# Performance work log

Measured on AMD Instinct MI355X. Metric: run time of the kernel, lower is better.

Reference implementation:

```python
import jax, jax.numpy as jnp
import numpy as np

S, B, D, H, F = 2048, 4, 256, 8, 2048
HD = D // H


def _ln(x, g, b, eps=1e-5):
    mu = jnp.mean(x, axis=-1, keepdims=True)
    var = jnp.var(x, axis=-1, keepdims=True)
    return (x - mu) * jax.lax.rsqrt(var + eps) * g + b


def setup_inputs() -> dict:
    key = jax.random.key(0)
    ks = jax.random.split(key, 8)
    s = lambda fan: 1.0 / np.sqrt(fan)
    return {
        "features": jax.random.normal(ks[0], (S, B, D), jnp.float32),
        "ln_g": jnp.ones((D,), jnp.float32),
        "ln_b": jnp.zeros((D,), jnp.float32),
        "in_proj_w": jax.random.normal(ks[1], (3 * D, D), jnp.float32) * s(D),
        "in_proj_b": jnp.zeros((3 * D,), jnp.float32),
        "out_proj_w": jax.random.normal(ks[2], (D, D), jnp.float32) * s(D),
        "out_proj_b": jnp.zeros((D,), jnp.float32),
        "w1": jax.random.normal(ks[3], (F, D), jnp.float32) * s(D),
        "b1": jnp.zeros((F,), jnp.float32),
        "w2": jax.random.normal(ks[4], (D, F), jnp.float32) * s(F),
        "b2": jnp.zeros((D,), jnp.float32),
    }


def _attn_tanh_relu(x, in_proj_w, in_proj_b, out_proj_w, out_proj_b):
    # x: (S, B, D). Standard MHA projections, but relu(tanh(.)) replaces softmax.
    qkv = x @ in_proj_w.T + in_proj_b            # (S, B, 3D)
    q, k, v = jnp.split(qkv, 3, axis=-1)
    q = q.reshape(S, B, H, HD) * (1.0 / np.sqrt(HD))
    k = k.reshape(S, B, H, HD)
    v = v.reshape(S, B, H, HD)
    scores = jnp.einsum("sbhd,tbhd->bhst", q, k)  # (B, H, S, S)
    w = jax.nn.relu(jnp.tanh(scores))
    out = jnp.einsum("bhst,tbhd->sbhd", w, v).reshape(S, B, D)
    return out @ out_proj_w.T + out_proj_b


def reference(features, ln_g, ln_b, in_proj_w, in_proj_b, out_proj_w, out_proj_b, w1, b1, w2, b2):
    ln_x = _ln(features, ln_g, ln_b)
    attn = _attn_tanh_relu(ln_x, in_proj_w, in_proj_b, out_proj_w, out_proj_b)
    r1 = _ln(ln_x + attn, ln_g, ln_b)
    ff = jax.nn.relu(r1 @ w1.T + b1) @ w2.T + b2
    return _ln(r1 + ff, ln_g, ln_b)
```

## Files before the change

kernel.cpp:

```cpp
#include <hip/hip_runtime.h>
#include <hip/hip_bf16.h>

#define SS 2048
#define BB 4
#define DD 256
#define HH 8
#define HDD 32
#define FFD 2048
#define MM (SS*BB)

typedef __attribute__((ext_vector_type(8))) __bf16 bf16x8;
typedef __attribute__((ext_vector_type(2))) __bf16 bf16x2;
typedef __attribute__((ext_vector_type(8))) short short8;
typedef __attribute__((ext_vector_type(4))) short short4v;
typedef __attribute__((ext_vector_type(4))) float f32x4;
typedef __attribute__((ext_vector_type(16))) float f32x16;
typedef __attribute__((ext_vector_type(2))) unsigned uint2v;
typedef __attribute__((ext_vector_type(4))) unsigned uint4v;

__device__ __forceinline__ unsigned short f2bf(float f) {
  union { float f; unsigned u; } v; v.f = f;
  unsigned r = v.u + 0x7fffu + ((v.u >> 16) & 1u);
  return (unsigned short)(r >> 16);
}

__device__ __forceinline__ unsigned pk2(float a, float b) {
  bf16x2 t; t[0] = (__bf16)a; t[1] = (__bf16)b;
  return __builtin_bit_cast(unsigned, t);
}

__device__ __forceinline__ void gload16(const void* g, void* l) {
  __builtin_amdgcn_global_load_lds(
      (const __attribute__((address_space(1))) void*)g,
      (__attribute__((address_space(3))) void*)l, 16, 0, 0);
}

__global__ __launch_bounds__(256)
void cvt_all(const float* __restrict__ a, const float* __restrict__ b,
             const float* __restrict__ c, const float* __restrict__ d,
             short* __restrict__ oa, short* __restrict__ ob,
             short* __restrict__ oc, short* __restrict__ od) {
  const int which = blockIdx.y;
  const float* in; short* out; int n4;
  if (which == 0)      { in = a; out = oa; n4 = 768 * 256 / 4; }
  else if (which == 1) { in = b; out = ob; n4 = 256 * 256 / 4; }
  else if (which == 2) { in = c; out = oc; n4 = 2048 * 256 / 4; }
  else                 { in = d; out = od; n4 = 2048 * 256 / 4; }
  const int i = blockIdx.x * 256 + threadIdx.x;
  if (i < n4) {
    float4 x = ((const float4*)in)[i];
    short4v o = { (short)f2bf(x.x), (short)f2bf(x.y), (short)f2bf(x.z), (short)f2bf(x.w) };
    ((short4v*)out)[i] = o;
  }
}

template<int NIN, int WF, int WBF>
__global__ __launch_bounds__(256)
void ln_kernel(const float* __restrict__ xa, const float* __restrict__ xb,
               const float* __restrict__ xc,
               const float* __restrict__ gam, const float* __restrict__ bet,
               float* __restrict__ outf, short* __restrict__ outb)
{
  const int w = threadIdx.x >> 6, l = threadIdx.x & 63;
  const size_t row = (size_t)blockIdx.x * 4 + w;
  float4 x = *(const float4*)&xa[row * 256 + l * 4];
  if (NIN >= 2) {
    const float4 y = *(const float4*)&xb[row * 256 + l * 4];
    x.x += y.x; x.y += y.y; x.z += y.z; x.w += y.w;
  }
  if (NIN >= 3) {
    const float4 y = *(const float4*)&xc[row * 256 + l * 4];
    x.x += y.x; x.y += y.y; x.z += y.z; x.w += y.w;
  }
  float sum = x.x + x.y + x.z + x.w;
  float sq  = x.x*x.x + x.y*x.y + x.z*x.z + x.w*x.w;
#pragma unroll
  for (int off = 32; off > 0; off >>= 1) {
    sum += __shfl_xor(sum, off);
    sq  += __shfl_xor(sq, off);
  }
  const float mu = sum * (1.f / 256.f);
  const float rs = rsqrtf(sq * (1.f / 256.f) - mu * mu + 1e-5f);
  const float4 g4 = *(const float4*)&gam[l * 4];
  const float4 b4 = *(const float4*)&bet[l * 4];
  const float y0 = (x.x - mu) * rs * g4.x + b4.x;
  const float y1 = (x.y - mu) * rs * g4.y + b4.y;
  const float y2 = (x.z - mu) * rs * g4.z + b4.z;
  const float y3 = (x.w - mu) * rs * g4.w + b4.w;
  if (WF) {
    float4 o; o.x = y0; o.y = y1; o.z = y2; o.w = y3;
    *(float4*)&outf[row * 256 + l * 4] = o;
  }
  if (WBF) {
    short4v o = { (short)f2bf(y0), (short)f2bf(y1), (short)f2bf(y2), (short)f2bf(y3) };
    *(short4v*)&outb[row * 256 + l * 4] = o;
  }
}

template<int EPI, int BM, int BN, int KW>
__global__ __launch_bounds__(256)
void gemm_bt(const short* __restrict__ A, const short* __restrict__ W,
             const float* __restrict__ bias, void* __restrict__ out,
             void* __restrict__ out2, int K, int N, int Ksub)
{
  __shared__ short sA[2][BM * 64];
  __shared__ short sB[2][BN * 64];
  const int tid = threadIdx.x;
  const int l  = tid & 63;
  const int w  = tid >> 6;
  const int wr = w >> 1, wc = w & 1;
  const int lr = l & 15, lg = l >> 4;
  const long row0 = (long)blockIdx.y * BM;
  const long col0 = (long)blockIdx.x * BN;
  const int kz = blockIdx.z;
  const int kbeg = kz * Ksub;
  const int ldsw = (tid & ~63) * 16;
  constexpr int MR = BM / 32, NR = BN / 32;
  f32x4 acc[MR][NR] = {};
  const int nt = Ksub / 64;

  auto stage = [&](int buf, int k0) {
#pragma unroll
    for (int i = 0; i < BM / 32; i++) {
      const int o = (i * 256 + tid) * 16;
      const int r = o >> 7;
      const int cg = ((o >> 4) & 7) ^ (r & 7);
      gload16((const char*)A + ((row0 + r) * (long)K + k0) * 2 + cg * 16,
              (char*)sA[buf] + i * 4096 + ldsw);
    }
    const long wstride = KW ? KW : K;
    const long wk = KW ? (k0 & (KW - 1)) : k0;
#pragma unroll
    for (int i = 0; i < BN / 32; i++) {
      const int o = (i * 256 + tid) * 16;
      const int r = o >> 7;
      const int cg = ((o >> 4) & 7) ^ (r & 7);
      gload16((const char*)W + ((col0 + r) * wstride + wk) * 2 + cg * 16,
              (char*)sB[buf] + i * 4096 + ldsw);
    }
  };

  stage(0, kbeg);
  __syncthreads();
  int cur = 0;
  for (int t = 0; t < nt; t++) {
    if (t + 1 < nt) stage(cur ^ 1, kbeg + (t + 1) * 64);
    bf16x8 af[MR][2], bw[NR][2];
#pragma unroll
    for (int m = 0; m < MR; m++)
#pragma unroll
      for (int kk = 0; kk < 2; kk++) {
        const int row = wr * (BM/2) + m * 16 + lr;
        af[m][kk] = *(const bf16x8*)&sA[cur][row * 64 + (((kk*4 + lg) ^ (lr & 7)) * 8)];
      }
#pragma unroll
    for (int n = 0; n < NR; n++)
#pragma unroll
      for (int kk = 0; kk < 2; kk++) {
        const int row = wc * (BN/2) + n * 16 + lr;
        bw[n][kk] = *(const bf16x8*)&sB[cur][row * 64 + (((kk*4 + lg) ^ (lr & 7)) * 8)];
      }
#pragma unroll
    for (int kk = 0; kk < 2; kk++)
#pragma unroll
      for (int m = 0; m < MR; m++)
#pragma unroll
        for (int n = 0; n < NR; n++)
          acc[m][n] = __builtin_amdgcn_mfma_f32_16x16x32_bf16(af[m][kk], bw[n][kk], acc[m][n], 0, 0, 0);
    __syncthreads();
    cur ^= 1;
  }

#pragma unroll
  for (int m = 0; m < MR; m++) {
    const long rbase = row0 + wr * (BM/2) + m * 16 + lg * 4;
#pragma unroll
    for (int n = 0; n < NR; n++) {
      const long c = col0 + wc * (BN/2) + n * 16 + lr;
      const float bv = (EPI == 3 && kz) ? 0.f : bias[c];
#pragma unroll
      for (int j = 0; j < 4; j++) {
        const long r = rbase + j;
        float val = acc[m][n][j] + bv;
        if (EPI == 0) {
          const int part = (int)(c >> 8);
          const int cc = (int)(c & 255);
          const int h = cc >> 5, hd = cc & 31;
          const int bi = (int)(r & 3);
          const int s = (int)(r >> 2);
          const int bh = bi * HH + h;
          if (part == 0) val *= 0.51006972771029396f;
          size_t idx;
          if (part == 2) {
            idx = (size_t)2 * (MM * DD) + (size_t)bh * (SS * HDD)
                + (size_t)(s >> 3) * (HDD * 8) + hd * 8 + (s & 7);
          } else {
            idx = (size_t)part * (MM * DD) + ((size_t)bh * SS + s) * HDD + hd;
          }
          ((short*)out)[idx] = (short)f2bf(val);
        } else if (EPI == 1) {
          ((float*)out)[(size_t)r * N + c] = val;
        } else if (EPI == 2) {
          ((short*)out)[(size_t)r * N + c] = (short)f2bf(fmaxf(val, 0.f));
        } else {
          float* op = kz ? (float*)out2 : (float*)out;
          op[(size_t)r * N + c] = val;
        }
      }
    }
  }
}

__global__ __launch_bounds__(256, 4)
void attn_kernel(const short* __restrict__ Qb, const short* __restrict__ Kb,
                 const short* __restrict__ Vb, short* __restrict__ Aout)
{
  const int tid = threadIdx.x;
  const int l = tid & 63, w = tid >> 6;
  const int q32 = l & 31, hf = l >> 5;
  const int i = blockIdx.x;
  const int j = i >> 3;
  const int p = (i & 7) + 8 * (j >> 6);
  const int rem = j & 63;
  const int q0 = (rem >> 2) * 128 + w * 32;
  const int kz = rem & 3;
  const int kbeg = kz * (SS / 4);
  const int kend = kbeg + SS / 4;
  const size_t base = (size_t)p * SS * HDD;
  const short* Q  = Qb + base;
  const short* Kp = Kb + base;
  const short* Vp = Vb + base;

  const short* qrow = &Q[(size_t)(q0 + q32) * HDD];
  const bf16x8 qf0 = *(const bf16x8*)&qrow[hf * 8];
  const bf16x8 qf1 = *(const bf16x8*)&qrow[16 + hf * 8];

  const f32x16 fzero = {};
  f32x16 accA = {}, accB = {};

  auto loadK = [&](int t0, bf16x8* kf) {
    const short* kr = &Kp[(size_t)(t0 + q32) * HDD];
    kf[0] = *(const bf16x8*)&kr[hf * 8];
    kf[1] = *(const bf16x8*)&kr[16 + hf * 8];
  };
  auto loadV = [&](int t0, bf16x8* vf) {
    const short* vb = &Vp[(size_t)((t0 >> 3) + hf) * (HDD * 8) + q32 * 8];
    vf[0] = *(const bf16x8*)&vb[0];
    vf[1] = *(const bf16x8*)&vb[2 * (HDD * 8)];
  };

  auto step = [&](const bf16x8* kf, const bf16x8* vf, f32x16& acc) {
    f32x16 s = __builtin_amdgcn_mfma_f32_32x32x16_bf16(kf[0], qf0, fzero, 0, 0, 0);
    s = __builtin_amdgcn_mfma_f32_32x32x16_bf16(kf[1], qf1, s, 0, 0, 0);
    float pv[16];
#pragma unroll
    for (int r = 0; r < 16; r++) {
      const float e = __builtin_amdgcn_exp2f(s[r]);
      pv[r] = fmaxf(1.f - 2.f * __builtin_amdgcn_rcpf(e + 1.f), 0.f);
    }
    unsigned X0 = pk2(pv[0], pv[1]),   X1 = pk2(pv[2], pv[3]);
    unsigned X2 = pk2(pv[4], pv[5]),   X3 = pk2(pv[6], pv[7]);
    unsigned X4 = pk2(pv[8], pv[9]),   X5 = pk2(pv[10], pv[11]);
    unsigned X6 = pk2(pv[12], pv[13]), X7 = pk2(pv[14], pv[15]);
    uint2v r02 = __builtin_amdgcn_permlane32_swap(X0, X2, false, false);
    uint2v r13 = __builtin_amdgcn_permlane32_swap(X1, X3, false, false);
    uint2v r46 = __builtin_amdgcn_permlane32_swap(X4, X6, false, false);
    uint2v r57 = __builtin_amdgcn_permlane32_swap(X5, X7, false, false);
    const uint4v f0 = { r02[0], r13[0], r02[1], r13[1] };
    const uint4v f1 = { r46[0], r57[0], r46[1], r57[1] };
    const bf16x8 pa0 = __builtin_bit_cast(bf16x8, f0);
    const bf16x8 pa1 = __builtin_bit_cast(bf16x8, f1);
    acc = __builtin_amdgcn_mfma_f32_32x32x16_bf16(pa0, vf[0], acc, 0, 0, 0);
    acc = __builtin_amdgcn_mfma_f32_32x32x16_bf16(pa1, vf[1], acc, 0, 0, 0);
  };

  bf16x8 kA[2], vA[2], kB[2], vB[2];
  loadK(kbeg, kA); loadV(kbeg, vA);
  for (int t0 = kbeg; t0 < kend; t0 += 64) {
    loadK(t0 + 32, kB); loadV(t0 + 32, vB);
    step(kA, vA, accA);
    const int tn = (t0 + 64 < kend) ? t0 + 64 : kbeg;
    loadK(tn, kA); loadV(tn, vA);
    step(kB, vB, accB);
  }

  const int bi = p >> 3, hh = p & 7;
  const size_t colo = (size_t)kz * DD + (size_t)hh * HDD + q32;
#pragma unroll
  for (int r = 0; r < 16; r++) {
    const int crow = (r & 3) + 8 * (r >> 2) + 4 * hf;
    Aout[((size_t)(q0 + crow) * BB + bi) * (4 * DD) + colo] =
        (short)f2bf(accA[r] + accB[r]);
  }
}

extern "C" void kernel_launch(void* const* d_in, const int* in_sizes, int n_in,
                              void* d_out, int out_size, void* d_ws, size_t ws_size,
                              hipStream_t stream) {
  const float* features   = (const float*)d_in[0];
  const float* ln_g       = (const float*)d_in[1];
  const float* ln_b       = (const float*)d_in[2];
  const float* in_proj_w  = (const float*)d_in[3];
  const float* in_proj_b  = (const float*)d_in[4];
  const float* out_proj_w = (const float*)d_in[5];
  const float* out_proj_b = (const float*)d_in[6];
  const float* w1 = (const float*)d_in[7];
  const float* b1 = (const float*)d_in[8];
  const float* w2 = (const float*)d_in[9];
  const float* b2 = (const float*)d_in[10];

  char* ws = (char*)d_ws;
  const size_t MB = 1024 * 1024;
  float* lnx_f  = (float*)(ws + 0);
  short* lnx_b  = (short*)(ws + 8 * MB);
  short* qkv    = (short*)(ws + 12 * MB);
  short* aprt   = (short*)(ws + 24 * MB);
  float* proj   = (float*)(ws + 12 * MB);
  short* r1_b   = (short*)(ws + 20 * MB);
  float* r1_f   = (float*)(ws + 24 * MB);
  short* h1     = (short*)(ws + 32 * MB);
  float* ffb    = (float*)(ws + 12 * MB);
  float* ffp1   = (float*)(ws + 0);
  short* wqkv_b = (short*)(ws + 64 * MB);
  short* wout_b = wqkv_b + 768 * 256;
  short* w1_b   = wout_b + 256 * 256;
  short* w2_b   = w1_b + 2048 * 256;

  cvt_all<<<dim3(512, 4), 256, 0, stream>>>(in_proj_w, out_proj_w, w1, w2,
                                            wqkv_b, wout_b, w1_b, w2_b);

  ln_kernel<1, 1, 1><<<2048, 256, 0, stream>>>(features, nullptr, nullptr, ln_g, ln_b, lnx_f, lnx_b);

  gemm_bt<0, 128, 64, 0><<<dim3(12, 64, 1), 256, 0, stream>>>(lnx_b, wqkv_b, in_proj_b, qkv, nullptr, 256, 768, 256);

  attn_kernel<<<dim3(2048, 1, 1), 256, 0, stream>>>(qkv, qkv + 2097152, qkv + 2 * 2097152, aprt);

  gemm_bt<1, 64, 64, 256><<<dim3(4, 128, 1), 256, 0, stream>>>(aprt, wout_b, out_proj_b, proj, nullptr, 1024, 256, 1024);

  ln_kernel<2, 1, 1><<<2048, 256, 0, stream>>>(lnx_f, proj, nullptr, ln_g, ln_b, r1_f, r1_b);

  gemm_bt<2, 128, 128, 0><<<dim3(16, 64, 1), 256, 0, stream>>>(r1_b, w1_b, b1, h1, nullptr, 256, 2048, 256);

  gemm_bt<3, 128, 64, 0><<<dim3(4, 64, 2), 256, 0, stream>>>(h1, w2_b, b2, ffb, ffp1, 2048, 256, 1024);

  ln_kernel<3, 1, 0><<<2048, 256, 0, stream>>>(r1_f, ffb, ffp1, ln_g, ln_b, (float*)d_out, nullptr);
}
```

Before: 132.0 us.

## Fuse weight conversion with first LayerNorm, halve attention key split, bf16 FFN partials

Merges the weight-conversion kernel and the first LayerNorm into one launch, removing a kernel boundary. The attention key-split factor drops from 4 to 2, which halves the partial-output buffer and the K dimension of the out-projection GEMM. The second FFN GEMM now writes its split-K partials as bf16 instead of fp32, and the final LayerNorm reads them as bf16. This cuts memory traffic and launch overhead, at the cost of fewer attention blocks (less parallelism) and extra bf16 rounding on the FFN partial sums.

```diff
diff --git a/kernel.cpp b/kernel.cpp
--- a/kernel.cpp
+++ b/kernel.cpp
@@ -24,6 +24,12 @@
   return (unsigned short)(r >> 16);
 }
 
+__device__ __forceinline__ float bf2f(short s) {
+  union { float f; unsigned u; } v;
+  v.u = ((unsigned)(unsigned short)s) << 16;
+  return v.f;
+}
+
 __device__ __forceinline__ unsigned pk2(float a, float b) {
   bf16x2 t; t[0] = (__bf16)a; t[1] = (__bf16)b;
   return __builtin_bit_cast(unsigned, t);
@@ -36,28 +42,57 @@
 }
 
 __global__ __launch_bounds__(256)
-void cvt_all(const float* __restrict__ a, const float* __restrict__ b,
-             const float* __restrict__ c, const float* __restrict__ d,
-             short* __restrict__ oa, short* __restrict__ ob,
-             short* __restrict__ oc, short* __restrict__ od) {
-  const int which = blockIdx.y;
-  const float* in; short* out; int n4;
-  if (which == 0)      { in = a; out = oa; n4 = 768 * 256 / 4; }
-  else if (which == 1) { in = b; out = ob; n4 = 256 * 256 / 4; }
-  else if (which == 2) { in = c; out = oc; n4 = 2048 * 256 / 4; }
-  else                 { in = d; out = od; n4 = 2048 * 256 / 4; }
-  const int i = blockIdx.x * 256 + threadIdx.x;
-  if (i < n4) {
-    float4 x = ((const float4*)in)[i];
-    short4v o = { (short)f2bf(x.x), (short)f2bf(x.y), (short)f2bf(x.z), (short)f2bf(x.w) };
-    ((short4v*)out)[i] = o;
-  }
-}
-
-template<int NIN, int WF, int WBF>
+void cvt_ln(const float* __restrict__ a, const float* __restrict__ b,
+            const float* __restrict__ c, const float* __restrict__ d,
+            short* __restrict__ oa, short* __restrict__ ob,
+            short* __restrict__ oc, short* __restrict__ od,
+            const float* __restrict__ feat,
+            const float* __restrict__ gam, const float* __restrict__ bet,
+            float* __restrict__ lnf, short* __restrict__ lnb)
+{
+  const int y = blockIdx.y;
+  if (y < 4) {
+    const float* in; short* out; int n4;
+    if (y == 0)      { in = a; out = oa; n4 = 768 * 256 / 4; }
+    else if (y == 1) { in = b; out = ob; n4 = 256 * 256 / 4; }
+    else if (y == 2) { in = c; out = oc; n4 = 2048 * 256 / 4; }
+    else             { in = d; out = od; n4 = 2048 * 256 / 4; }
+    const int i = blockIdx.x * 256 + threadIdx.x;
+    if (i < n4) {
+      float4 x = ((const float4*)in)[i];
+      short4v o = { (short)f2bf(x.x), (short)f2bf(x.y), (short)f2bf(x.z), (short)f2bf(x.w) };
+      ((short4v*)out)[i] = o;
+    }
+    return;
+  }
+  const int w = threadIdx.x >> 6, l = threadIdx.x & 63;
+  const size_t row = (size_t)blockIdx.x * 4 + w;
+  float4 x = *(const float4*)&feat[row * 256 + l * 4];
+  float sum = x.x + x.y + x.z + x.w;
+  float sq  = x.x*x.x + x.y*x.y + x.z*x.z + x.w*x.w;
+#pragma unroll
+  for (int off = 32; off > 0; off >>= 1) {
+    sum += __shfl_xor(sum, off);
+    sq  += __shfl_xor(sq, off);
+  }
+  const float mu = sum * (1.f / 256.f);
+  const float rs = rsqrtf(sq * (1.f / 256.f) - mu * mu + 1e-5f);
+  const float4 g4 = *(const float4*)&gam[l * 4];
+  const float4 b4 = *(const float4*)&bet[l * 4];
+  const float y0 = (x.x - mu) * rs * g4.x + b4.x;
+  const float y1 = (x.y - mu) * rs * g4.y + b4.y;
+  const float y2 = (x.z - mu) * rs * g4.z + b4.z;
+  const float y3 = (x.w - mu) * rs * g4.w + b4.w;
+  float4 o; o.x = y0; o.y = y1; o.z = y2; o.w = y3;
+  *(float4*)&lnf[row * 256 + l * 4] = o;
+  short4v ob2 = { (short)f2bf(y0), (short)f2bf(y1), (short)f2bf(y2), (short)f2bf(y3) };
+  *(short4v*)&lnb[row * 256 + l * 4] = ob2;
+}
+
+template<int NIN, int WF, int WBF, int BFI>
 __global__ __launch_bounds__(256)
-void ln_kernel(const float* __restrict__ xa, const float* __restrict__ xb,
-               const float* __restrict__ xc,
+void ln_kernel(const float* __restrict__ xa, const void* __restrict__ xb,
+               const void* __restrict__ xc,
                const float* __restrict__ gam, const float* __restrict__ bet,
                float* __restrict__ outf, short* __restrict__ outb)
 {
@@ -65,12 +100,22 @@
   const size_t row = (size_t)blockIdx.x * 4 + w;
   float4 x = *(const float4*)&xa[row * 256 + l * 4];
   if (NIN >= 2) {
-    const float4 y = *(const float4*)&xb[row * 256 + l * 4];
-    x.x += y.x; x.y += y.y; x.z += y.z; x.w += y.w;
+    if (BFI) {
+      const short4v yb = *(const short4v*)&((const short*)xb)[row * 256 + l * 4];
+      x.x += bf2f(yb[0]); x.y += bf2f(yb[1]); x.z += bf2f(yb[2]); x.w += bf2f(yb[3]);
+    } else {
+      const float4 yv = *(const float4*)&((const float*)xb)[row * 256 + l * 4];
+      x.x += yv.x; x.y += yv.y; x.z += yv.z; x.w += yv.w;
+    }
   }
   if (NIN >= 3) {
-    const float4 y = *(const float4*)&xc[row * 256 + l * 4];
-    x.x += y.x; x.y += y.y; x.z += y.z; x.w += y.w;
+    if (BFI) {
+      const short4v yc = *(const short4v*)&((const short*)xc)[row * 256 + l * 4];
+      x.x += bf2f(yc[0]); x.y += bf2f(yc[1]); x.z += bf2f(yc[2]); x.w += bf2f(yc[3]);
+    } else {
+      const float4 yv = *(const float4*)&((const float*)xc)[row * 256 + l * 4];
+      x.x += yv.x; x.y += yv.y; x.z += yv.z; x.w += yv.w;
+    }
   }
   float sum = x.x + x.y + x.z + x.w;
   float sq  = x.x*x.x + x.y*x.y + x.z*x.z + x.w*x.w;
@@ -203,8 +248,8 @@
         } else if (EPI == 2) {
           ((short*)out)[(size_t)r * N + c] = (short)f2bf(fmaxf(val, 0.f));
         } else {
-          float* op = kz ? (float*)out2 : (float*)out;
-          op[(size_t)r * N + c] = val;
+          short* op = kz ? (short*)out2 : (short*)out;
+          op[(size_t)r * N + c] = (short)f2bf(val);
         }
       }
     }
@@ -220,12 +265,12 @@
   const int q32 = l & 31, hf = l >> 5;
   const int i = blockIdx.x;
   const int j = i >> 3;
-  const int p = (i & 7) + 8 * (j >> 6);
-  const int rem = j & 63;
-  const int q0 = (rem >> 2) * 128 + w * 32;
-  const int kz = rem & 3;
-  const int kbeg = kz * (SS / 4);
-  const int kend = kbeg + SS / 4;
+  const int p = (i & 7) + 8 * (j >> 5);
+  const int rem = j & 31;
+  const int q0 = (rem >> 1) * 128 + w * 32;
+  const int kz = rem & 1;
+  const int kbeg = kz * (SS / 2);
+  const int kend = kbeg + SS / 2;
   const size_t base = (size_t)p * SS * HDD;
   const short* Q  = Qb + base;
   const short* Kp = Kb + base;
@@ -289,7 +334,7 @@
 #pragma unroll
   for (int r = 0; r < 16; r++) {
     const int crow = (r & 3) + 8 * (r >> 2) + 4 * hf;
-    Aout[((size_t)(q0 + crow) * BB + bi) * (4 * DD) + colo] =
+    Aout[((size_t)(q0 + crow) * BB + bi) * (2 * DD) + colo] =
         (short)f2bf(accA[r] + accB[r]);
   }
 }
@@ -319,29 +364,28 @@
   short* r1_b   = (short*)(ws + 20 * MB);
   float* r1_f   = (float*)(ws + 24 * MB);
   short* h1     = (short*)(ws + 32 * MB);
-  float* ffb    = (float*)(ws + 12 * MB);
-  float* ffp1   = (float*)(ws + 0);
+  short* ffb    = (short*)(ws + 12 * MB);
+  short* ffp1   = (short*)(ws + 16 * MB);
   short* wqkv_b = (short*)(ws + 64 * MB);
   short* wout_b = wqkv_b + 768 * 256;
   short* w1_b   = wout_b + 256 * 256;
   short* w2_b   = w1_b + 2048 * 256;
 
-  cvt_all<<<dim3(512, 4), 256, 0, stream>>>(in_proj_w, out_proj_w, w1, w2,
-                                            wqkv_b, wout_b, w1_b, w2_b);
-
-  ln_kernel<1, 1, 1><<<2048, 256, 0, stream>>>(features, nullptr, nullptr, ln_g, ln_b, lnx_f, lnx_b);
+  cvt_ln<<<dim3(2048, 5), 256, 0, stream>>>(in_proj_w, out_proj_w, w1, w2,
+                                            wqkv_b, wout_b, w1_b, w2_b,
+                                            features, ln_g, ln_b, lnx_f, lnx_b);
 
   gemm_bt<0, 128, 64, 0><<<dim3(12, 64, 1), 256, 0, stream>>>(lnx_b, wqkv_b, in_proj_b, qkv, nullptr, 256, 768, 256);
 
-  attn_kernel<<<dim3(2048, 1, 1), 256, 0, stream>>>(qkv, qkv + 2097152, qkv + 2 * 2097152, aprt);
-
-  gemm_bt<1, 64, 64, 256><<<dim3(4, 128, 1), 256, 0, stream>>>(aprt, wout_b, out_proj_b, proj, nullptr, 1024, 256, 1024);
-
-  ln_kernel<2, 1, 1><<<2048, 256, 0, stream>>>(lnx_f, proj, nullptr, ln_g, ln_b, r1_f, r1_b);
+  attn_kernel<<<dim3(1024, 1, 1), 256, 0, stream>>>(qkv, qkv + 2097152, qkv + 2 * 2097152, aprt);
+
+  gemm_bt<1, 64, 64, 256><<<dim3(4, 128, 1), 256, 0, stream>>>(aprt, wout_b, out_proj_b, proj, nullptr, 512, 256, 512);
+
+  ln_kernel<2, 1, 1, 0><<<2048, 256, 0, stream>>>(lnx_f, proj, nullptr, ln_g, ln_b, r1_f, r1_b);
 
   gemm_bt<2, 128, 128, 0><<<dim3(16, 64, 1), 256, 0, stream>>>(r1_b, w1_b, b1, h1, nullptr, 256, 2048, 256);
 
   gemm_bt<3, 128, 64, 0><<<dim3(4, 64, 2), 256, 0, stream>>>(h1, w2_b, b2, ffb, ffp1, 2048, 256, 1024);
 
-  ln_kernel<3, 1, 0><<<2048, 256, 0, stream>>>(r1_f, ffb, ffp1, ln_g, ln_b, (float*)d_out, nullptr);
-}
+  ln_kernel<3, 1, 0, 1><<<2048, 256, 0, stream>>>(r1_f, ffb, ffp1, ln_g, ln_b, (float*)d_out, nullptr);
+}
```

After: 124.7 us (median of 2 runs). 5.5% less time.
